# Kernel tuning notes

Hardware: AMD Instinct MI355X
Metric: run time of the kernel (lower is better)

Reference implementation:

```python
import jax, jax.numpy as jnp
import numpy as np

N_SRC = 50000
N_DST = 50000
N_EDGES = 800000
D = 128
H = 128


def setup_inputs() -> dict:
    key = jax.random.key(0)
    ks = jax.random.split(key, 10)
    return {
        "feat_src": jax.random.normal(ks[0], (N_SRC, D), dtype=jnp.float32),
        "feat_dst": jax.random.normal(ks[1], (N_DST, D), dtype=jnp.float32),
        "W1": jax.random.normal(ks[2], (H, D), dtype=jnp.float32) * 0.05,
        "b1": jnp.zeros((H,), dtype=jnp.float32),
        "W2": jax.random.normal(ks[3], (H, 3 * D), dtype=jnp.float32) * 0.05,
        "b2": jnp.zeros((H,), dtype=jnp.float32),
        "W3": jax.random.normal(ks[4], (H, 2 * H), dtype=jnp.float32) * 0.05,
        "b3": jnp.zeros((H,), dtype=jnp.float32),
        "src_idx": jax.random.randint(ks[5], (N_EDGES,), 0, N_SRC, dtype=jnp.int32),
        "dst_idx": jax.random.randint(ks[6], (N_EDGES,), 0, N_DST, dtype=jnp.int32),
    }


def reference(feat_src, feat_dst, W1, b1, W2, b2, W3, b3, src_idx, dst_idx):
    n_dst = feat_dst.shape[0]
    # copy_u: gather source features along edges  [E, D]
    m = feat_src[src_idx]
    # fn.max -> 'max'; NOTE: source code's 'mean' is ALSO fn.max (faithful to bug)
    mx = jax.ops.segment_max(m, dst_idx, num_segments=n_dst)
    mx = jnp.where(jnp.isfinite(mx), mx, jnp.zeros_like(mx))  # zero-degree dst -> 0 (DGL convention)
    sm = jax.ops.segment_sum(m, dst_idx, num_segments=n_dst)
    agg = jnp.concatenate([mx, mx, sm], axis=1)  # [N_dst, 3D]
    z2 = agg @ W2.T + b2            # fc2
    z1 = feat_dst @ W1.T + b1       # fc1
    h = jax.nn.relu(jnp.concatenate([z2, z1], axis=1))  # [N_dst, 2H]
    out = jax.nn.relu(h @ W3.T + b3)  # fc3 = Linear + ReLU
    return out
```

## Files before the change

kernel.cpp:

```cpp
#include <hip/hip_runtime.h>
#include <math.h>

#define NDST 50000
#define NSRC 50000
#define NEDGE 800000
#define DF 128

#define NBUK 1563
#define NCH 128
#define EPC (NEDGE / NCH)
#define HN (NBUK * NCH)
#define CAP 1536

typedef __attribute__((ext_vector_type(4))) float f32x4;
typedef __attribute__((ext_vector_type(8))) short bf16x8;

__device__ __forceinline__ ushort f2bf(float f) {
    union { float f; unsigned int u; } c; c.f = f;
    unsigned int u = c.u;
    unsigned int r = (u + 0x7fffu + ((u >> 16) & 1u)) >> 16;
    return (ushort)r;
}
__device__ __forceinline__ float bflo(unsigned int u) {
    union { unsigned int u; float f; } c; c.u = u << 16; return c.f;
}
__device__ __forceinline__ float bfhi(unsigned int u) {
    union { unsigned int u; float f; } c; c.u = u & 0xffff0000u; return c.f;
}

#define NB_CONV 6250
#define NB_ZERO 196
#define NB_PREP 320

__global__ void prep_all(const float* __restrict__ fs, unsigned int* __restrict__ fs_b,
                         uint4* __restrict__ hist4,
                         const float* __restrict__ W2, const float* __restrict__ W1,
                         const float* __restrict__ W3,
                         ushort* __restrict__ Wz_b, ushort* __restrict__ W1_b,
                         ushort* __restrict__ W3_b) {
    int b = blockIdx.x, tid = threadIdx.x;
    if (b < NB_CONV) {
        int i = b * 256 + tid;
        float4 v = *(const float4*)(fs + (size_t)i * 4);
        unsigned int lo = (unsigned int)f2bf(v.x) | ((unsigned int)f2bf(v.y) << 16);
        unsigned int hi = (unsigned int)f2bf(v.z) | ((unsigned int)f2bf(v.w) << 16);
        *(uint2*)(fs_b + (size_t)i * 2) = make_uint2(lo, hi);
    } else if (b < NB_CONV + NB_ZERO) {
        int i = (b - NB_CONV) * 256 + tid;
        if (i < HN / 4) hist4[i] = make_uint4(0, 0, 0, 0);
    } else {
        int i = (b - NB_CONV - NB_ZERO) * 256 + tid;
        if (i < 128 * 256) {
            int c = i >> 8, k = i & 255;
            float v = (k < 128) ? (W2[c * 384 + k] + W2[c * 384 + 128 + k])
                                : W2[c * 384 + 128 + k];
            Wz_b[i] = f2bf(v);
        } else if (i < 128 * 256 + 128 * 128) {
            int j = i - 128 * 256;
            W1_b[j] = f2bf(W1[j]);
        } else if (i < 128 * 256 + 128 * 128 + 128 * 256) {
            int j = i - 128 * 256 - 128 * 128;
            W3_b[j] = f2bf(W3[j]);
        }
    }
}

__global__ void hist_k(const int* __restrict__ dst_idx, int* __restrict__ hist) {
    int c = blockIdx.x, tid = threadIdx.x;
    int base = c * EPC;
    for (int e = base + tid; e < base + EPC; e += 256)
        atomicAdd(&hist[(dst_idx[e] >> 5) * NCH + c], 1);
}

__global__ void scan_bsums(const int* __restrict__ a, int* __restrict__ bsum, int n) {
    __shared__ int ws[4];
    int i = blockIdx.x * 256 + threadIdx.x;
    int v = (i < n) ? a[i] : 0;
    #pragma unroll
    for (int off = 32; off > 0; off >>= 1) v += __shfl_down(v, off, 64);
    if ((threadIdx.x & 63) == 0) ws[threadIdx.x >> 6] = v;
    __syncthreads();
    if (threadIdx.x == 0) bsum[blockIdx.x] = ws[0] + ws[1] + ws[2] + ws[3];
}

__global__ __launch_bounds__(256)
void scan_mid(const int* __restrict__ bsum, int* __restrict__ bpre, int nb) {
    __shared__ int part[256];
    int t = threadIdx.x;
    int ch = (nb + 255) / 256;
    int lo = t * ch, hi = min(nb, lo + ch);
    int s = 0;
    for (int i = lo; i < hi; ++i) s += bsum[i];
    part[t] = s;
    __syncthreads();
    for (int off = 1; off < 256; off <<= 1) {
        int v = (t >= off) ? part[t - off] : 0;
        __syncthreads();
        part[t] += v;
        __syncthreads();
    }
    int run = (t == 0) ? 0 : part[t - 1];
    for (int i = lo; i < hi; ++i) { bpre[i] = run; run += bsum[i]; }
}

__global__ __launch_bounds__(256)
void scan_final(const int* __restrict__ a, const int* __restrict__ bpre,
                int* __restrict__ out, int n) {
    __shared__ int s[256];
    int b = blockIdx.x, t = threadIdx.x;
    int i = b * 256 + t;
    int v = (i < n) ? a[i] : 0;
    s[t] = v;
    __syncthreads();
    for (int off = 1; off < 256; off <<= 1) {
        int u = (t >= off) ? s[t - off] : 0;
        __syncthreads();
        s[t] += u;
        __syncthreads();
    }
    if (i < n) out[i] = bpre[b] + s[t] - v;
}

__global__ __launch_bounds__(256)
void partition_k(const int* __restrict__ src_idx, const int* __restrict__ dst_idx,
                 const int* __restrict__ scanned, unsigned int* __restrict__ pairs) {
    __shared__ int offs_l[NBUK];
    int c = blockIdx.x, tid = threadIdx.x;
    for (int i = tid; i < NBUK; i += 256) offs_l[i] = scanned[i * NCH + c];
    __syncthreads();
    int base = c * EPC;
    for (int e = base + tid; e < base + EPC; e += 256) {
        int d = dst_idx[e];
        int pos = atomicAdd(&offs_l[d >> 5], 1);
        pairs[pos] = (unsigned int)src_idx[e] | ((unsigned int)(d & 31) << 16);
    }
}

__global__ __launch_bounds__(256)
void bucket_sort_agg(const unsigned int* __restrict__ fs_b,
                     const unsigned int* __restrict__ pairs,
                     const int* __restrict__ scanned,
                     unsigned int* __restrict__ mx_b, unsigned int* __restrict__ sm_b) {
    __shared__ int s_src[CAP];
    __shared__ int s_cnt[32], s_off[32], s_cur[32];
    int B = blockIdx.x, tid = threadIdx.x;
    int w = tid >> 6, lane = tid & 63;
    int s0 = scanned[B * NCH];
    int s1 = (B + 1 < NBUK) ? scanned[(B + 1) * NCH] : NEDGE;

    float mx0[8], mx1[8], sm0[8], sm1[8];
    #pragma unroll
    for (int j = 0; j < 8; ++j) {
        mx0[j] = -INFINITY; mx1[j] = -INFINITY; sm0[j] = 0.f; sm1[j] = 0.f;
    }

    for (int cs = s0; cs < s1; cs += CAP) {
        int n = min(CAP, s1 - cs);
        if (tid < 32) s_cnt[tid] = 0;
        __syncthreads();
        for (int i = tid; i < n; i += 256)
            atomicAdd(&s_cnt[(pairs[cs + i] >> 16) & 31u], 1);
        __syncthreads();
        if (tid < 32) {
            int v = s_cnt[tid];
            int incl = v;
            #pragma unroll
            for (int d = 1; d < 32; d <<= 1) {
                int o = __shfl_up(incl, d, 64);
                if (tid >= d) incl += o;
            }
            s_off[tid] = incl - v;
            s_cur[tid] = incl - v;
        }
        __syncthreads();
        for (int i = tid; i < n; i += 256) {
            unsigned int p = pairs[cs + i];
            int pos = atomicAdd(&s_cur[(p >> 16) & 31u], 1);
            s_src[pos] = (int)(p & 0xFFFFu);
        }
        __syncthreads();
        #pragma unroll
        for (int j = 0; j < 8; ++j) {
            int dl = w * 8 + j;
            int e = s_off[dl], eend = e + s_cnt[dl];
            for (; e + 3 < eend; e += 4) {
                int i0 = s_src[e], i1 = s_src[e + 1], i2 = s_src[e + 2], i3 = s_src[e + 3];
                unsigned int u0 = fs_b[(size_t)i0 * 64 + lane];
                unsigned int u1 = fs_b[(size_t)i1 * 64 + lane];
                unsigned int u2 = fs_b[(size_t)i2 * 64 + lane];
                unsigned int u3 = fs_b[(size_t)i3 * 64 + lane];
                float a0 = bflo(u0), c0 = bfhi(u0);
                float a1 = bflo(u1), c1 = bfhi(u1);
                float a2 = bflo(u2), c2 = bfhi(u2);
                float a3 = bflo(u3), c3 = bfhi(u3);
                mx0[j] = fmaxf(fmaxf(fmaxf(mx0[j], a0), a1), fmaxf(a2, a3));
                mx1[j] = fmaxf(fmaxf(fmaxf(mx1[j], c0), c1), fmaxf(c2, c3));
                sm0[j] += (a0 + a1) + (a2 + a3);
                sm1[j] += (c0 + c1) + (c2 + c3);
            }
            for (; e < eend; ++e) {
                unsigned int u = fs_b[(size_t)s_src[e] * 64 + lane];
                float a = bflo(u), c = bfhi(u);
                mx0[j] = fmaxf(mx0[j], a);
                mx1[j] = fmaxf(mx1[j], c);
                sm0[j] += a;
                sm1[j] += c;
            }
        }
        __syncthreads();
    }

    int base_d = B * 32;
    #pragma unroll
    for (int j = 0; j < 8; ++j) {
        int d = base_d + w * 8 + j;
        if (d >= NDST) continue;
        float m0 = mx0[j], m1 = mx1[j];
        if (m0 == -INFINITY) m0 = 0.f;
        if (m1 == -INFINITY) m1 = 0.f;
        union { float f; unsigned int u; } c0, c1;
        c0.f = m0; c1.f = m1;
        size_t o = (size_t)d * 64 + lane;
        mx_b[o] = (c0.u >> 16) | (c1.u & 0xFFFF0000u);
        sm_b[o] = (unsigned int)f2bf(sm0[j]) | ((unsigned int)f2bf(sm1[j]) << 16);
    }
}

#define BM2 64
#define LDW 40
#define LDH 264

__global__ __launch_bounds__(256)
void mlp_fused(const ushort* __restrict__ mxa, const ushort* __restrict__ sma,
               const float* __restrict__ feat_dst,
               const ushort* __restrict__ Wz_b, const ushort* __restrict__ W1_b,
               const ushort* __restrict__ W3_b,
               const float* __restrict__ b1, const float* __restrict__ b2,
               const float* __restrict__ b3,
               float* __restrict__ out) {
    __shared__ ushort Hs[BM2 * LDH];
    __shared__ ushort As[BM2 * LDW];
    __shared__ ushort Ws[128 * LDW];
    int tid = threadIdx.x;
    int bm = blockIdx.x * BM2;
    int wid = tid >> 6, lane = tid & 63;
    int wm = (wid & 1) * 32, wn = (wid >> 1) * 64;
    int lrow = lane & 15, lk8 = (lane >> 4) * 8;
    int rbase = (lane >> 4) * 4;

    int sra = tid >> 2, ska = (tid & 3) * 8;
    int srw = tid >> 1, skw = (tid & 1) * 16;

    f32x4 acc[2][4];

    #pragma unroll
    for (int half = 0; half < 2; ++half) {
        #pragma unroll
        for (int i = 0; i < 2; ++i)
            #pragma unroll
            for (int j = 0; j < 4; ++j)
                acc[i][j] = (f32x4){0.f, 0.f, 0.f, 0.f};
        int K = half ? 128 : 256;
        const ushort* Wb = half ? W1_b : Wz_b;
        for (int k0 = 0; k0 < K; k0 += 32) {
            int m = bm + sra;
            uint4 av = make_uint4(0, 0, 0, 0);
            if (m < NDST) {
                if (half == 0) {
                    const ushort* ap = (k0 < 128) ? mxa : sma;
                    av = *(const uint4*)(ap + (size_t)m * 128 + (k0 & 127) + ska);
                } else {
                    const float* p = feat_dst + (size_t)m * 128 + k0 + ska;
                    unsigned int pk[4];
                    #pragma unroll
                    for (int j = 0; j < 4; ++j) {
                        float x = p[2 * j], y = p[2 * j + 1];
                        pk[j] = (unsigned int)f2bf(x) | ((unsigned int)f2bf(y) << 16);
                    }
                    av = make_uint4(pk[0], pk[1], pk[2], pk[3]);
                }
            }
            *(uint4*)&As[sra * LDW + ska] = av;

            const ushort* wp = Wb + (size_t)srw * K + k0 + skw;
            *(uint4*)&Ws[srw * LDW + skw] = *(const uint4*)wp;
            *(uint4*)&Ws[srw * LDW + skw + 8] = *(const uint4*)(wp + 8);
            __syncthreads();

            bf16x8 af[2], bfr[4];
            #pragma unroll
            for (int mi = 0; mi < 2; ++mi)
                af[mi] = *(const bf16x8*)&As[(wm + mi * 16 + lrow) * LDW + lk8];
            #pragma unroll
            for (int ni = 0; ni < 4; ++ni)
                bfr[ni] = *(const bf16x8*)&Ws[(wn + ni * 16 + lrow) * LDW + lk8];
            #pragma unroll
            for (int mi = 0; mi < 2; ++mi)
                #pragma unroll
                for (int ni = 0; ni < 4; ++ni)
                    acc[mi][ni] = __builtin_amdgcn_mfma_f32_16x16x32_bf16(
                        af[mi], bfr[ni], acc[mi][ni], 0, 0, 0);
            __syncthreads();
        }
        const float* bias = half ? b1 : b2;
        #pragma unroll
        for (int ni = 0; ni < 4; ++ni) {
            int n = wn + ni * 16 + lrow;
            float bv = bias[n];
            #pragma unroll
            for (int mi = 0; mi < 2; ++mi)
                #pragma unroll
                for (int r = 0; r < 4; ++r) {
                    float v = fmaxf(acc[mi][ni][r] + bv, 0.f);
                    Hs[(wm + mi * 16 + rbase + r) * LDH + half * 128 + n] = f2bf(v);
                }
        }
    }
    __syncthreads();

    #pragma unroll
    for (int i = 0; i < 2; ++i)
        #pragma unroll
        for (int j = 0; j < 4; ++j)
            acc[i][j] = (f32x4){0.f, 0.f, 0.f, 0.f};
    for (int k0 = 0; k0 < 256; k0 += 32) {
        const ushort* wp = W3_b + (size_t)srw * 256 + k0 + skw;
        *(uint4*)&Ws[srw * LDW + skw] = *(const uint4*)wp;
        *(uint4*)&Ws[srw * LDW + skw + 8] = *(const uint4*)(wp + 8);
        __syncthreads();

        bf16x8 af[2], bfr[4];
        #pragma unroll
        for (int mi = 0; mi < 2; ++mi)
            af[mi] = *(const bf16x8*)&Hs[(wm + mi * 16 + lrow) * LDH + k0 + lk8];
        #pragma unroll
        for (int ni = 0; ni < 4; ++ni)
            bfr[ni] = *(const bf16x8*)&Ws[(wn + ni * 16 + lrow) * LDW + lk8];
        #pragma unroll
        for (int mi = 0; mi < 2; ++mi)
            #pragma unroll
            for (int ni = 0; ni < 4; ++ni)
                acc[mi][ni] = __builtin_amdgcn_mfma_f32_16x16x32_bf16(
                    af[mi], bfr[ni], acc[mi][ni], 0, 0, 0);
        __syncthreads();
    }
    #pragma unroll
    for (int ni = 0; ni < 4; ++ni) {
        int n = wn + ni * 16 + lrow;
        float bv = b3[n];
        #pragma unroll
        for (int mi = 0; mi < 2; ++mi)
            #pragma unroll
            for (int r = 0; r < 4; ++r) {
                int m = bm + wm + mi * 16 + rbase + r;
                if (m < NDST)
                    out[(size_t)m * 128 + n] = fmaxf(acc[mi][ni][r] + bv, 0.f);
            }
    }
}

extern "C" void kernel_launch(void* const* d_in, const int* in_sizes, int n_in,
                              void* d_out, int out_size, void* d_ws, size_t ws_size,
                              hipStream_t stream) {
    const float* feat_src = (const float*)d_in[0];
    const float* feat_dst = (const float*)d_in[1];
    const float* W1 = (const float*)d_in[2];
    const float* b1 = (const float*)d_in[3];
    const float* W2 = (const float*)d_in[4];
    const float* b2 = (const float*)d_in[5];
    const float* W3 = (const float*)d_in[6];
    const float* b3 = (const float*)d_in[7];
    const int* src_idx = (const int*)d_in[8];
    const int* dst_idx = (const int*)d_in[9];

    float* out = (float*)d_out;

    unsigned int* fs_b = (unsigned int*)d_ws;
    unsigned int* mx_b = fs_b + (size_t)NSRC * 64;
    unsigned int* sm_b = mx_b + (size_t)NDST * 64;
    ushort* Wz_b = (ushort*)(sm_b + (size_t)NDST * 64);
    ushort* W1_b = Wz_b + 128 * 256;
    ushort* W3_b = W1_b + 128 * 128;
    int* hist    = (int*)(W3_b + 128 * 256);
    int* scanned = hist + HN;
    int* bsum    = scanned + HN;
    int* bpre    = bsum + 1024;
    unsigned int* pairs = (unsigned int*)(bpre + 1024);

    const int NBH = (HN + 255) / 256;

    prep_all<<<NB_CONV + NB_ZERO + NB_PREP, 256, 0, stream>>>(
        feat_src, fs_b, (uint4*)hist, W2, W1, W3, Wz_b, W1_b, W3_b);

    hist_k<<<NCH, 256, 0, stream>>>(dst_idx, hist);
    scan_bsums<<<NBH, 256, 0, stream>>>(hist, bsum, HN);
    scan_mid<<<1, 256, 0, stream>>>(bsum, bpre, NBH);
    scan_final<<<NBH, 256, 0, stream>>>(hist, bpre, scanned, HN);
    partition_k<<<NCH, 256, 0, stream>>>(src_idx, dst_idx, scanned, pairs);

    bucket_sort_agg<<<NBUK, 256, 0, stream>>>(fs_b, pairs, scanned, mx_b, sm_b);

    mlp_fused<<<(NDST + BM2 - 1) / BM2, 256, 0, stream>>>(
        (const ushort*)mx_b, (const ushort*)sm_b, feat_dst,
        Wz_b, W1_b, W3_b, b1, b2, b3, out);
}
```

Measured before the change: 146.6 us.

## Load MLP operands directly from global memory and pre-convert feat_dst to bf16

The fused MLP kernel drops its shared-memory staging of A and W tiles, along with the per-step barriers. Each wave now loads its MFMA fragments straight from global memory, and only the hidden layer stays in LDS, with the row pitch changed from 264 to 260. feat_dst is converted to bf16 in the prep kernel so the MLP reads half the bytes and does no conversion inline. The cost is an extra full pass over feat_dst (read fp32, write bf16), and weight fragments are fetched redundantly per wave, relying on L2/L1 caching.

```diff
diff --git a/kernel.cpp b/kernel.cpp
--- a/kernel.cpp
+++ b/kernel.cpp
@@ -29,27 +29,31 @@
 }
 
 #define NB_CONV 6250
+#define NB_CONVD 6250
 #define NB_ZERO 196
 #define NB_PREP 320
 
 __global__ void prep_all(const float* __restrict__ fs, unsigned int* __restrict__ fs_b,
+                         const float* __restrict__ fd, unsigned int* __restrict__ fd_b,
                          uint4* __restrict__ hist4,
                          const float* __restrict__ W2, const float* __restrict__ W1,
                          const float* __restrict__ W3,
                          ushort* __restrict__ Wz_b, ushort* __restrict__ W1_b,
                          ushort* __restrict__ W3_b) {
     int b = blockIdx.x, tid = threadIdx.x;
-    if (b < NB_CONV) {
-        int i = b * 256 + tid;
-        float4 v = *(const float4*)(fs + (size_t)i * 4);
+    if (b < NB_CONV + NB_CONVD) {
+        const float* src = (b < NB_CONV) ? fs : fd;
+        unsigned int* dst = (b < NB_CONV) ? fs_b : fd_b;
+        int i = ((b < NB_CONV) ? b : b - NB_CONV) * 256 + tid;
+        float4 v = *(const float4*)(src + (size_t)i * 4);
         unsigned int lo = (unsigned int)f2bf(v.x) | ((unsigned int)f2bf(v.y) << 16);
         unsigned int hi = (unsigned int)f2bf(v.z) | ((unsigned int)f2bf(v.w) << 16);
-        *(uint2*)(fs_b + (size_t)i * 2) = make_uint2(lo, hi);
-    } else if (b < NB_CONV + NB_ZERO) {
-        int i = (b - NB_CONV) * 256 + tid;
+        *(uint2*)(dst + (size_t)i * 2) = make_uint2(lo, hi);
+    } else if (b < NB_CONV + NB_CONVD + NB_ZERO) {
+        int i = (b - NB_CONV - NB_CONVD) * 256 + tid;
         if (i < HN / 4) hist4[i] = make_uint4(0, 0, 0, 0);
     } else {
-        int i = (b - NB_CONV - NB_ZERO) * 256 + tid;
+        int i = (b - NB_CONV - NB_CONVD - NB_ZERO) * 256 + tid;
         if (i < 128 * 256) {
             int c = i >> 8, k = i & 255;
             float v = (k < 128) ? (W2[c * 384 + k] + W2[c * 384 + 128 + k])
@@ -227,20 +231,17 @@
 }
 
 #define BM2 64
-#define LDW 40
-#define LDH 264
+#define LDH 260
 
 __global__ __launch_bounds__(256)
 void mlp_fused(const ushort* __restrict__ mxa, const ushort* __restrict__ sma,
-               const float* __restrict__ feat_dst,
+               const ushort* __restrict__ fdb,
                const ushort* __restrict__ Wz_b, const ushort* __restrict__ W1_b,
                const ushort* __restrict__ W3_b,
                const float* __restrict__ b1, const float* __restrict__ b2,
                const float* __restrict__ b3,
                float* __restrict__ out) {
     __shared__ ushort Hs[BM2 * LDH];
-    __shared__ ushort As[BM2 * LDW];
-    __shared__ ushort Ws[128 * LDW];
     int tid = threadIdx.x;
     int bm = blockIdx.x * BM2;
     int wid = tid >> 6, lane = tid & 63;
@@ -248,113 +249,95 @@
     int lrow = lane & 15, lk8 = (lane >> 4) * 8;
     int rbase = (lane >> 4) * 4;
 
-    int sra = tid >> 2, ska = (tid & 3) * 8;
-    int srw = tid >> 1, skw = (tid & 1) * 16;
+    int am0 = min(bm + wm + lrow, NDST - 1);
+    int am1 = min(bm + wm + 16 + lrow, NDST - 1);
+    int bn[4];
+    #pragma unroll
+    for (int ni = 0; ni < 4; ++ni) bn[ni] = wn + ni * 16 + lrow;
 
     f32x4 acc[2][4];
 
     #pragma unroll
-    for (int half = 0; half < 2; ++half) {
-        #pragma unroll
-        for (int i = 0; i < 2; ++i)
-            #pragma unroll
-            for (int j = 0; j < 4; ++j)
-                acc[i][j] = (f32x4){0.f, 0.f, 0.f, 0.f};
-        int K = half ? 128 : 256;
-        const ushort* Wb = half ? W1_b : Wz_b;
-        for (int k0 = 0; k0 < K; k0 += 32) {
-            int m = bm + sra;
-            uint4 av = make_uint4(0, 0, 0, 0);
-            if (m < NDST) {
-                if (half == 0) {
-                    const ushort* ap = (k0 < 128) ? mxa : sma;
-                    av = *(const uint4*)(ap + (size_t)m * 128 + (k0 & 127) + ska);
-                } else {
-                    const float* p = feat_dst + (size_t)m * 128 + k0 + ska;
-                    unsigned int pk[4];
-                    #pragma unroll
-                    for (int j = 0; j < 4; ++j) {
-                        float x = p[2 * j], y = p[2 * j + 1];
-                        pk[j] = (unsigned int)f2bf(x) | ((unsigned int)f2bf(y) << 16);
-                    }
-                    av = make_uint4(pk[0], pk[1], pk[2], pk[3]);
-                }
-            }
-            *(uint4*)&As[sra * LDW + ska] = av;
-
-            const ushort* wp = Wb + (size_t)srw * K + k0 + skw;
-            *(uint4*)&Ws[srw * LDW + skw] = *(const uint4*)wp;
-            *(uint4*)&Ws[srw * LDW + skw + 8] = *(const uint4*)(wp + 8);
-            __syncthreads();
-
-            bf16x8 af[2], bfr[4];
-            #pragma unroll
-            for (int mi = 0; mi < 2; ++mi)
-                af[mi] = *(const bf16x8*)&As[(wm + mi * 16 + lrow) * LDW + lk8];
-            #pragma unroll
-            for (int ni = 0; ni < 4; ++ni)
-                bfr[ni] = *(const bf16x8*)&Ws[(wn + ni * 16 + lrow) * LDW + lk8];
-            #pragma unroll
-            for (int mi = 0; mi < 2; ++mi)
-                #pragma unroll
-                for (int ni = 0; ni < 4; ++ni)
-                    acc[mi][ni] = __builtin_amdgcn_mfma_f32_16x16x32_bf16(
-                        af[mi], bfr[ni], acc[mi][ni], 0, 0, 0);
-            __syncthreads();
-        }
-        const float* bias = half ? b1 : b2;
+    for (int i = 0; i < 2; ++i)
+        #pragma unroll
+        for (int j = 0; j < 4; ++j) acc[i][j] = (f32x4){0.f, 0.f, 0.f, 0.f};
+    #pragma unroll 2
+    for (int k0 = 0; k0 < 256; k0 += 32) {
+        const ushort* ap = (k0 < 128) ? mxa : sma;
+        int kl = (k0 & 127) + lk8;
+        bf16x8 af0 = *(const bf16x8*)(ap + (size_t)am0 * 128 + kl);
+        bf16x8 af1 = *(const bf16x8*)(ap + (size_t)am1 * 128 + kl);
         #pragma unroll
         for (int ni = 0; ni < 4; ++ni) {
-            int n = wn + ni * 16 + lrow;
-            float bv = bias[n];
-            #pragma unroll
-            for (int mi = 0; mi < 2; ++mi)
-                #pragma unroll
-                for (int r = 0; r < 4; ++r) {
-                    float v = fmaxf(acc[mi][ni][r] + bv, 0.f);
-                    Hs[(wm + mi * 16 + rbase + r) * LDH + half * 128 + n] = f2bf(v);
-                }
-        }
-    }
-    __syncthreads();
-
-    #pragma unroll
-    for (int i = 0; i < 2; ++i)
-        #pragma unroll
-        for (int j = 0; j < 4; ++j)
-            acc[i][j] = (f32x4){0.f, 0.f, 0.f, 0.f};
-    for (int k0 = 0; k0 < 256; k0 += 32) {
-        const ushort* wp = W3_b + (size_t)srw * 256 + k0 + skw;
-        *(uint4*)&Ws[srw * LDW + skw] = *(const uint4*)wp;
-        *(uint4*)&Ws[srw * LDW + skw + 8] = *(const uint4*)(wp + 8);
-        __syncthreads();
-
-        bf16x8 af[2], bfr[4];
-        #pragma unroll
-        for (int mi = 0; mi < 2; ++mi)
-            af[mi] = *(const bf16x8*)&Hs[(wm + mi * 16 + lrow) * LDH + k0 + lk8];
-        #pragma unroll
-        for (int ni = 0; ni < 4; ++ni)
-            bfr[ni] = *(const bf16x8*)&Ws[(wn + ni * 16 + lrow) * LDW + lk8];
+            bf16x8 bf = *(const bf16x8*)(Wz_b + (size_t)bn[ni] * 256 + k0 + lk8);
+            acc[0][ni] = __builtin_amdgcn_mfma_f32_16x16x32_bf16(af0, bf, acc[0][ni], 0, 0, 0);
+            acc[1][ni] = __builtin_amdgcn_mfma_f32_16x16x32_bf16(af1, bf, acc[1][ni], 0, 0, 0);
+        }
+    }
+    #pragma unroll
+    for (int ni = 0; ni < 4; ++ni) {
+        float bv = b2[bn[ni]];
         #pragma unroll
         for (int mi = 0; mi < 2; ++mi)
             #pragma unroll
-            for (int ni = 0; ni < 4; ++ni)
-                acc[mi][ni] = __builtin_amdgcn_mfma_f32_16x16x32_bf16(
-                    af[mi], bfr[ni], acc[mi][ni], 0, 0, 0);
-        __syncthreads();
+            for (int r = 0; r < 4; ++r)
+                Hs[(wm + mi * 16 + rbase + r) * LDH + bn[ni]] =
+                    f2bf(fmaxf(acc[mi][ni][r] + bv, 0.f));
+    }
+
+    #pragma unroll
+    for (int i = 0; i < 2; ++i)
+        #pragma unroll
+        for (int j = 0; j < 4; ++j) acc[i][j] = (f32x4){0.f, 0.f, 0.f, 0.f};
+    #pragma unroll 2
+    for (int k0 = 0; k0 < 128; k0 += 32) {
+        bf16x8 af0 = *(const bf16x8*)(fdb + (size_t)am0 * 128 + k0 + lk8);
+        bf16x8 af1 = *(const bf16x8*)(fdb + (size_t)am1 * 128 + k0 + lk8);
+        #pragma unroll
+        for (int ni = 0; ni < 4; ++ni) {
+            bf16x8 bf = *(const bf16x8*)(W1_b + (size_t)bn[ni] * 128 + k0 + lk8);
+            acc[0][ni] = __builtin_amdgcn_mfma_f32_16x16x32_bf16(af0, bf, acc[0][ni], 0, 0, 0);
+            acc[1][ni] = __builtin_amdgcn_mfma_f32_16x16x32_bf16(af1, bf, acc[1][ni], 0, 0, 0);
+        }
     }
     #pragma unroll
     for (int ni = 0; ni < 4; ++ni) {
-        int n = wn + ni * 16 + lrow;
-        float bv = b3[n];
+        float bv = b1[bn[ni]];
+        #pragma unroll
+        for (int mi = 0; mi < 2; ++mi)
+            #pragma unroll
+            for (int r = 0; r < 4; ++r)
+                Hs[(wm + mi * 16 + rbase + r) * LDH + 128 + bn[ni]] =
+                    f2bf(fmaxf(acc[mi][ni][r] + bv, 0.f));
+    }
+
+    __syncthreads();
+
+    #pragma unroll
+    for (int i = 0; i < 2; ++i)
+        #pragma unroll
+        for (int j = 0; j < 4; ++j) acc[i][j] = (f32x4){0.f, 0.f, 0.f, 0.f};
+    #pragma unroll 2
+    for (int k0 = 0; k0 < 256; k0 += 32) {
+        bf16x8 af0 = *(const bf16x8*)&Hs[(wm + lrow) * LDH + k0 + lk8];
+        bf16x8 af1 = *(const bf16x8*)&Hs[(wm + 16 + lrow) * LDH + k0 + lk8];
+        #pragma unroll
+        for (int ni = 0; ni < 4; ++ni) {
+            bf16x8 bf = *(const bf16x8*)(W3_b + (size_t)bn[ni] * 256 + k0 + lk8);
+            acc[0][ni] = __builtin_amdgcn_mfma_f32_16x16x32_bf16(af0, bf, acc[0][ni], 0, 0, 0);
+            acc[1][ni] = __builtin_amdgcn_mfma_f32_16x16x32_bf16(af1, bf, acc[1][ni], 0, 0, 0);
+        }
+    }
+    #pragma unroll
+    for (int ni = 0; ni < 4; ++ni) {
+        float bv = b3[bn[ni]];
         #pragma unroll
         for (int mi = 0; mi < 2; ++mi)
             #pragma unroll
             for (int r = 0; r < 4; ++r) {
                 int m = bm + wm + mi * 16 + rbase + r;
                 if (m < NDST)
-                    out[(size_t)m * 128 + n] = fmaxf(acc[mi][ni][r] + bv, 0.f);
+                    out[(size_t)m * 128 + bn[ni]] = fmaxf(acc[mi][ni][r] + bv, 0.f);
             }
     }
 }
@@ -378,7 +361,8 @@
     unsigned int* fs_b = (unsigned int*)d_ws;
     unsigned int* mx_b = fs_b + (size_t)NSRC * 64;
     unsigned int* sm_b = mx_b + (size_t)NDST * 64;
-    ushort* Wz_b = (ushort*)(sm_b + (size_t)NDST * 64);
+    unsigned int* fd_b = sm_b + (size_t)NDST * 64;
+    ushort* Wz_b = (ushort*)(fd_b + (size_t)NDST * 64);
     ushort* W1_b = Wz_b + 128 * 256;
     ushort* W3_b = W1_b + 128 * 128;
     int* hist    = (int*)(W3_b + 128 * 256);
@@ -389,8 +373,8 @@
 
     const int NBH = (HN + 255) / 256;
 
-    prep_all<<<NB_CONV + NB_ZERO + NB_PREP, 256, 0, stream>>>(
-        feat_src, fs_b, (uint4*)hist, W2, W1, W3, Wz_b, W1_b, W3_b);
+    prep_all<<<NB_CONV + NB_CONVD + NB_ZERO + NB_PREP, 256, 0, stream>>>(
+        feat_src, fs_b, feat_dst, fd_b, (uint4*)hist, W2, W1, W3, Wz_b, W1_b, W3_b);
 
     hist_k<<<NCH, 256, 0, stream>>>(dst_idx, hist);
     scan_bsums<<<NBH, 256, 0, stream>>>(hist, bsum, HN);
@@ -401,6 +385,6 @@
     bucket_sort_agg<<<NBUK, 256, 0, stream>>>(fs_b, pairs, scanned, mx_b, sm_b);
 
     mlp_fused<<<(NDST + BM2 - 1) / BM2, 256, 0, stream>>>(
-        (const ushort*)mx_b, (const ushort*)sm_b, feat_dst,
+        (const ushort*)mx_b, (const ushort*)sm_b, (const ushort*)fd_b,
         Wz_b, W1_b, W3_b, b1, b2, b3, out);
 }
```

Result: slower. 168.2 us (+14.8%).
